# Kernel optimization log

Hardware: AMD Instinct MI355X
Metric: run time of the kernel (lower is better)

## Reference

```python
import jax, jax.numpy as jnp
import numpy as np

# SSMBlock constants (from init_kwargs and standard mamba_ssm defaults)
W = 8            # pooled spatial edge; d_model = W^3
K = 16           # AvgPool3d kernel & stride
D_MODEL = W ** 3            # 512
D_STATE = 16
EXPAND = 2
D_INNER = EXPAND * D_MODEL  # 1024
DT_RANK = D_MODEL // 16     # 32 (ceil(512/16))
D_CONV = 4


def setup_inputs() -> dict:
    key = jax.random.key(0)
    ks = jax.random.split(key, 8)
    s = 0.02
    x = jax.random.normal(ks[0], (1, 64, 128, 128, 128), dtype=jnp.float32)
    in_proj_w = jax.random.normal(ks[1], (2 * D_INNER, D_MODEL), jnp.float32) * s
    conv_w = jax.random.normal(ks[2], (D_INNER, D_CONV), jnp.float32) * s
    conv_b = jnp.zeros((D_INNER,), jnp.float32)
    x_proj_w = jax.random.normal(ks[3], (DT_RANK + 2 * D_STATE, D_INNER), jnp.float32) * s
    dt_proj_w = jax.random.normal(ks[4], (D_INNER, DT_RANK), jnp.float32) * s
    dt_proj_b = jax.random.uniform(ks[5], (D_INNER,), jnp.float32, minval=-4.0, maxval=-2.0)
    A_log = jnp.log(jnp.broadcast_to(jnp.arange(1, D_STATE + 1, dtype=jnp.float32), (D_INNER, D_STATE)))
    D = jnp.ones((D_INNER,), jnp.float32)
    out_proj_w = jax.random.normal(ks[6], (D_MODEL, D_INNER), jnp.float32) * s
    return dict(x=x, in_proj_w=in_proj_w, conv_w=conv_w, conv_b=conv_b,
                x_proj_w=x_proj_w, dt_proj_w=dt_proj_w, dt_proj_b=dt_proj_b,
                A_log=A_log, D=D, out_proj_w=out_proj_w)


def _forward(x, in_proj_w, conv_w, conv_b, x_proj_w, dt_proj_w, dt_proj_b, A_log, D, out_proj_w):
    B, C = x.shape[0], x.shape[1]
    # AvgPool3d(K, stride=K): non-overlapping -> reshape + mean
    xp = x.reshape(B, C, W, K, W, K, W, K).mean(axis=(3, 5, 7))  # (B,C,W,W,W)
    seq = xp.reshape(B, C, D_MODEL)  # Mamba input: L = C, d_model = W^3

    # in_proj -> (x, z)
    xz = jnp.einsum('bld,ed->ble', seq, in_proj_w)  # (B,L,2*D_INNER)
    xs, z = jnp.split(xz, 2, axis=-1)

    # causal depthwise conv1d along L + SiLU
    xt = jnp.pad(xs, ((0, 0), (D_CONV - 1, 0), (0, 0))).transpose(0, 2, 1)  # (B,E,L+pad)
    conv = jax.lax.conv_general_dilated(
        xt, conv_w[:, None, :], window_strides=(1,), padding='VALID',
        dimension_numbers=('NCH', 'OIH', 'NCH'), feature_group_count=D_INNER)
    xs = jax.nn.silu(conv.transpose(0, 2, 1) + conv_b)  # (B,L,E)

    # input-dependent dt, B, C
    x_dbl = jnp.einsum('ble,fe->blf', xs, x_proj_w)
    dt, Bs, Cs = jnp.split(x_dbl, [DT_RANK, DT_RANK + D_STATE], axis=-1)
    dt = jax.nn.softplus(jnp.einsum('blr,er->ble', dt, dt_proj_w) + dt_proj_b)  # (B,L,E)

    # selective scan: h_t = exp(dt*A) h_{t-1} + (dt*x) B_t ; y_t = <h_t, C_t> + D*x_t
    A = -jnp.exp(A_log)                                  # (E,S)
    dA = jnp.exp(dt[..., None] * A)                      # (B,L,E,S)
    dBx = (dt * xs)[..., None] * Bs[:, :, None, :]       # (B,L,E,S)

    def step(h, inp):
        da, dbx, c = inp
        h = da * h + dbx                                 # (B,E,S)
        y = jnp.einsum('bes,bs->be', h, c)
        return h, y

    h0 = jnp.zeros((B, D_INNER, D_STATE), xs.dtype)
    _, ys = jax.lax.scan(step, h0, (dA.transpose(1, 0, 2, 3), dBx.transpose(1, 0, 2, 3), Cs.transpose(1, 0, 2)))
    y = ys.transpose(1, 0, 2) + xs * D                   # (B,L,E)

    y = y * jax.nn.silu(z)
    out = jnp.einsum('ble,de->bld', y, out_proj_w)       # (B,L,d_model)
    return out.reshape(B, C, W, W, W)


def reference(x, in_proj_w, conv_w, conv_b, x_proj_w, dt_proj_w, dt_proj_b, A_log, D, out_proj_w):
    return _forward(x, in_proj_w, conv_w, conv_b, x_proj_w, dt_proj_w, dt_proj_b, A_log, D, out_proj_w)
```

## Files before the change

kernel.cpp:

```cpp
#include <hip/hip_runtime.h>
#include <math.h>

typedef float f32x4 __attribute__((ext_vector_type(4)));

__device__ __forceinline__ float dot4v(f32x4 a, f32x4 b){
    return a.x*b.x + a.y*b.y + a.z*b.z + a.w*b.w;
}
__device__ __forceinline__ float dot4(float4 a, float4 b){
    return a.x*b.x + a.y*b.y + a.z*b.z + a.w*b.w;
}

__device__ __forceinline__ float reduce4(float a0, float a1, float a2, float a3, int lane){
    int b0 = lane & 1, b1 = lane & 2;
    float r  = b0 ? a1 : a0;
    float rt = b0 ? a0 : a1;
    r += __shfl_xor(rt, 1);
    float s  = b0 ? a3 : a2;
    float st = b0 ? a2 : a3;
    s += __shfl_xor(st, 1);
    float u  = b1 ? s : r;
    float ut = b1 ? r : s;
    u += __shfl_xor(ut, 2);
    u += __shfl_xor(u, 4);
    u += __shfl_xor(u, 8);
    u += __shfl_xor(u, 16);
    u += __shfl_xor(u, 32);
    return u;
}

__global__ __launch_bounds__(256) void pool_k(const float* __restrict__ x,
                                              float* __restrict__ seqp){
    int tid  = threadIdx.x;
    int lane = tid & 63;
    int wid  = blockIdx.x * 4 + (tid >> 6);
    int part = wid & 3;
    int cdh  = wid >> 2;
    int c  = cdh >> 6;
    int od = (cdh >> 3) & 7;
    int oh = cdh & 7;
    int half = lane >> 5;
    int f    = lane & 31;

    const f32x4* px = (const f32x4*)x;
    size_t base = ((size_t)(c * 128 + od * 16) * 128 + (size_t)(oh * 16 + half)) * 32 + f
                + (size_t)part * 4 * 4096;

    float acc = 0.f;
    #pragma unroll
    for (int ii = 0; ii < 4; ii++){
        size_t o = base + (size_t)ii * 4096;
        #pragma unroll
        for (int jj = 0; jj < 8; jj++){
            f32x4 v = __builtin_nontemporal_load(&px[o + (size_t)jj * 64]);
            acc += (v.x + v.y) + (v.z + v.w);
        }
    }
    acc += __shfl_xor(acc, 1);
    acc += __shfl_xor(acc, 2);
    acc += __shfl_xor(acc, 32);
    if (lane < 32 && (lane & 3) == 0){
        int ow = lane >> 2;
        seqp[part * 32768 + c * 512 + od * 64 + oh * 8 + ow] = acc * (1.0f / 4096.0f);
    }
}

__device__ __forceinline__ f32x4 loadS(const f32x4* __restrict__ P, int row, int idx){
    f32x4 v = P[(size_t)row * 128 + idx];
    #pragma unroll
    for (int p = 1; p < 4; p++) v += P[(size_t)p * 8192 + (size_t)row * 128 + idx];
    return v;
}

__global__ __launch_bounds__(256) void inproj_k(const float* __restrict__ seqp,
                                                const float* __restrict__ Win,
                                                float* __restrict__ xz){
    int lane = threadIdx.x & 63;
    int wid  = blockIdx.x * 4 + (threadIdx.x >> 6);
    int l0 = (wid >> 7) << 2;
    int e0 = (wid & 127) << 4;
    const f32x4* P = (const f32x4*)seqp;
    f32x4 s0a = loadS(P, l0+0, lane), s0b = loadS(P, l0+0, lane + 64);
    f32x4 s1a = loadS(P, l0+1, lane), s1b = loadS(P, l0+1, lane + 64);
    f32x4 s2a = loadS(P, l0+2, lane), s2b = loadS(P, l0+2, lane + 64);
    f32x4 s3a = loadS(P, l0+3, lane), s3b = loadS(P, l0+3, lane + 64);
    #pragma unroll 4
    for (int j = 0; j < 16; j++){
        int e = e0 + j;
        const f32x4* W = (const f32x4*)Win + (size_t)e * 128;
        f32x4 w0 = W[lane], w1 = W[lane + 64];
        float a0 = dot4v(w0, s0a) + dot4v(w1, s0b);
        float a1 = dot4v(w0, s1a) + dot4v(w1, s1b);
        float a2 = dot4v(w0, s2a) + dot4v(w1, s2b);
        float a3 = dot4v(w0, s3a) + dot4v(w1, s3b);
        float u = reduce4(a0, a1, a2, a3, lane);
        if (lane < 4) xz[(size_t)(l0 + lane) * 2048 + e] = u;
    }
}

__global__ __launch_bounds__(256) void mid_k(const float* __restrict__ xz,
                                             const float* __restrict__ cw,
                                             const float* __restrict__ cb,
                                             const float* __restrict__ Wx,
                                             const float* __restrict__ Wdt,
                                             const float* __restrict__ bdt,
                                             float* __restrict__ xsT,
                                             float* __restrict__ zsT,
                                             float* __restrict__ dtT,
                                             float* __restrict__ bcT){
    __shared__ float xs_row[1024];
    __shared__ float xd_row[64];
    int l = blockIdx.x;
    int t = threadIdx.x;

    #pragma unroll
    for (int j = 0; j < 4; j++){
        int e = t + j * 256;
        float v = cb[e];
        #pragma unroll
        for (int tt = 0; tt < 4; tt++){
            int ll = l - 3 + tt;
            if (ll >= 0) v += cw[e * 4 + tt] * xz[(size_t)ll * 2048 + e];
        }
        v = v / (1.f + expf(-v));
        xs_row[e] = v;
        xsT[(size_t)e * 64 + l] = v;
        float zv = xz[(size_t)l * 2048 + 1024 + e];
        zsT[(size_t)e * 64 + l] = zv / (1.f + expf(-zv));
    }
    __syncthreads();

    {
        int f = t >> 2, q = t & 3;
        const float4* X  = (const float4*)xs_row;
        const float4* W4 = (const float4*)(Wx + (size_t)f * 1024);
        float acc = 0.f;
        #pragma unroll 8
        for (int k = 0; k < 64; k++){
            int idx = q * 64 + k;
            acc += dot4(X[idx], W4[idx]);
        }
        acc += __shfl_xor(acc, 1);
        acc += __shfl_xor(acc, 2);
        if (q == 0){
            xd_row[f] = acc;
            if (f >= 32) bcT[(size_t)(f - 32) * 64 + l] = acc;
        }
    }
    __syncthreads();

    #pragma unroll
    for (int j = 0; j < 4; j++){
        int e = t + j * 256;
        const float4* W4 = (const float4*)(Wdt + (size_t)e * 32);
        const float4* R  = (const float4*)xd_row;
        float acc = bdt[e];
        #pragma unroll
        for (int k4 = 0; k4 < 8; k4++) acc += dot4(R[k4], W4[k4]);
        float sp = (acc > 20.f) ? acc : log1pf(expf(acc));
        dtT[(size_t)e * 64 + l] = sp;
    }
}

__global__ __launch_bounds__(256) void scan_k(const float* __restrict__ dtT,
                                              const float* __restrict__ xsT,
                                              const float* __restrict__ zsT,
                                              const float* __restrict__ bcT,
                                              const float* __restrict__ A_log,
                                              const float* __restrict__ Dv,
                                              float* __restrict__ y){
    __shared__ float red[4][64];
    int e    = blockIdx.x;
    int lane = threadIdx.x & 63;
    int w    = threadIdx.x >> 6;

    float dtv = dtT[(size_t)e * 64 + lane];
    float xv  = xsT[(size_t)e * 64 + lane];

    float py = 0.f;
    #pragma unroll
    for (int i = 0; i < 4; i++){
        int s = w * 4 + i;
        float A = -expf(A_log[e * 16 + s]);
        float a = expf(dtv * A);
        float b = (dtv * xv) * bcT[s * 64 + lane];
        #pragma unroll
        for (int d = 1; d < 64; d <<= 1){
            float ap = __shfl_up(a, d);
            float bp = __shfl_up(b, d);
            if (lane >= d){ b += a * bp; a *= ap; }
        }
        py += b * bcT[(16 + s) * 64 + lane];
    }
    red[w][lane] = py;
    __syncthreads();
    if (threadIdx.x < 64){
        float tot = red[0][lane] + red[1][lane] + red[2][lane] + red[3][lane];
        float yv = (tot + xv * Dv[e]) * zsT[(size_t)e * 64 + lane];
        y[(size_t)lane * 1024 + e] = yv;
    }
}

__global__ __launch_bounds__(256) void outproj_k(const float* __restrict__ y,
                                                 const float* __restrict__ Wo,
                                                 float* __restrict__ out){
    int lane = threadIdx.x & 63;
    int wid  = blockIdx.x * 4 + (threadIdx.x >> 6);
    int l0 = (wid >> 5) << 2;
    int d0 = (wid & 31) << 4;
    const float4* Y = (const float4*)y;
    float4 y0[4], y1[4], y2[4], y3[4];
    #pragma unroll
    for (int q = 0; q < 4; q++){
        y0[q] = Y[(size_t)(l0+0)*256 + q*64 + lane];
        y1[q] = Y[(size_t)(l0+1)*256 + q*64 + lane];
        y2[q] = Y[(size_t)(l0+2)*256 + q*64 + lane];
        y3[q] = Y[(size_t)(l0+3)*256 + q*64 + lane];
    }
    #pragma unroll 2
    for (int j = 0; j < 16; j++){
        int d = d0 + j;
        const float4* W = (const float4*)Wo + (size_t)d * 256;
        float a0 = 0.f, a1 = 0.f, a2 = 0.f, a3 = 0.f;
        #pragma unroll
        for (int q = 0; q < 4; q++){
            float4 w = W[q * 64 + lane];
            a0 += dot4(w, y0[q]);
            a1 += dot4(w, y1[q]);
            a2 += dot4(w, y2[q]);
            a3 += dot4(w, y3[q]);
        }
        float u = reduce4(a0, a1, a2, a3, lane);
        if (lane < 4) out[(size_t)(l0 + lane) * 512 + d] = u;
    }
}

extern "C" void kernel_launch(void* const* d_in, const int* in_sizes, int n_in,
                              void* d_out, int out_size, void* d_ws, size_t ws_size,
                              hipStream_t stream){
    const float* x          = (const float*)d_in[0];
    const float* in_proj_w  = (const float*)d_in[1];
    const float* conv_w     = (const float*)d_in[2];
    const float* conv_b     = (const float*)d_in[3];
    const float* x_proj_w   = (const float*)d_in[4];
    const float* dt_proj_w  = (const float*)d_in[5];
    const float* dt_proj_b  = (const float*)d_in[6];
    const float* A_log      = (const float*)d_in[7];
    const float* Dv         = (const float*)d_in[8];
    const float* out_proj_w = (const float*)d_in[9];
    float* out = (float*)d_out;

    float* ws   = (float*)d_ws;
    float* seqp = ws;
    float* xz   = ws + 131072;
    float* xsT  = ws + 262144;
    float* zsT  = ws + 327680;
    float* dtT  = ws + 393216;
    float* bcT  = ws + 458752;
    float* y    = ws + 460800;

    hipLaunchKernelGGL(pool_k,    dim3(4096), dim3(256), 0, stream, x, seqp);
    hipLaunchKernelGGL(inproj_k,  dim3(512),  dim3(256), 0, stream, seqp, in_proj_w, xz);
    hipLaunchKernelGGL(mid_k,     dim3(64),   dim3(256), 0, stream, xz, conv_w, conv_b,
                       x_proj_w, dt_proj_w, dt_proj_b, xsT, zsT, dtT, bcT);
    hipLaunchKernelGGL(scan_k,    dim3(1024), dim3(256), 0, stream, dtT, xsT, zsT, bcT, A_log, Dv, y);
    hipLaunchKernelGGL(outproj_k, dim3(128),  dim3(256), 0, stream, y, out_proj_w, out);
}
```

Before: 134.7 us.

## Reduce pool partials in-block, widen inproj rows, move dt_proj into scan

```diff
diff --git a/kernel.cpp b/kernel.cpp
--- a/kernel.cpp
+++ b/kernel.cpp
@@ -29,12 +29,12 @@
 }
 
 __global__ __launch_bounds__(256) void pool_k(const float* __restrict__ x,
-                                              float* __restrict__ seqp){
+                                              float* __restrict__ seq){
+    __shared__ float red[4][8];
     int tid  = threadIdx.x;
     int lane = tid & 63;
-    int wid  = blockIdx.x * 4 + (tid >> 6);
-    int part = wid & 3;
-    int cdh  = wid >> 2;
+    int part = tid >> 6;
+    int cdh  = blockIdx.x;
     int c  = cdh >> 6;
     int od = (cdh >> 3) & 7;
     int oh = cdh & 7;
@@ -58,63 +58,59 @@
     acc += __shfl_xor(acc, 1);
     acc += __shfl_xor(acc, 2);
     acc += __shfl_xor(acc, 32);
-    if (lane < 32 && (lane & 3) == 0){
-        int ow = lane >> 2;
-        seqp[part * 32768 + c * 512 + od * 64 + oh * 8 + ow] = acc * (1.0f / 4096.0f);
-    }
-}
-
-__device__ __forceinline__ f32x4 loadS(const f32x4* __restrict__ P, int row, int idx){
-    f32x4 v = P[(size_t)row * 128 + idx];
-    #pragma unroll
-    for (int p = 1; p < 4; p++) v += P[(size_t)p * 8192 + (size_t)row * 128 + idx];
-    return v;
-}
-
-__global__ __launch_bounds__(256) void inproj_k(const float* __restrict__ seqp,
+    if (lane < 32 && (lane & 3) == 0) red[part][lane >> 2] = acc;
+    __syncthreads();
+    if (tid < 8){
+        float v = red[0][tid] + red[1][tid] + red[2][tid] + red[3][tid];
+        seq[c * 512 + od * 64 + oh * 8 + tid] = v * (1.0f / 4096.0f);
+    }
+}
+
+__global__ __launch_bounds__(256) void inproj_k(const float* __restrict__ seq,
                                                 const float* __restrict__ Win,
                                                 float* __restrict__ xz){
     int lane = threadIdx.x & 63;
     int wid  = blockIdx.x * 4 + (threadIdx.x >> 6);
-    int l0 = (wid >> 7) << 2;
+    int l0 = (wid >> 7) << 3;
     int e0 = (wid & 127) << 4;
-    const f32x4* P = (const f32x4*)seqp;
-    f32x4 s0a = loadS(P, l0+0, lane), s0b = loadS(P, l0+0, lane + 64);
-    f32x4 s1a = loadS(P, l0+1, lane), s1b = loadS(P, l0+1, lane + 64);
-    f32x4 s2a = loadS(P, l0+2, lane), s2b = loadS(P, l0+2, lane + 64);
-    f32x4 s3a = loadS(P, l0+3, lane), s3b = loadS(P, l0+3, lane + 64);
-    #pragma unroll 4
+    const f32x4* S = (const f32x4*)seq;
+    f32x4 sa[8], sb[8];
+    #pragma unroll
+    for (int r = 0; r < 8; r++){
+        sa[r] = S[(size_t)(l0 + r) * 128 + lane];
+        sb[r] = S[(size_t)(l0 + r) * 128 + lane + 64];
+    }
+    #pragma unroll 2
     for (int j = 0; j < 16; j++){
         int e = e0 + j;
         const f32x4* W = (const f32x4*)Win + (size_t)e * 128;
         f32x4 w0 = W[lane], w1 = W[lane + 64];
-        float a0 = dot4v(w0, s0a) + dot4v(w1, s0b);
-        float a1 = dot4v(w0, s1a) + dot4v(w1, s1b);
-        float a2 = dot4v(w0, s2a) + dot4v(w1, s2b);
-        float a3 = dot4v(w0, s3a) + dot4v(w1, s3b);
-        float u = reduce4(a0, a1, a2, a3, lane);
-        if (lane < 4) xz[(size_t)(l0 + lane) * 2048 + e] = u;
-    }
-}
-
-__global__ __launch_bounds__(256) void mid_k(const float* __restrict__ xz,
-                                             const float* __restrict__ cw,
-                                             const float* __restrict__ cb,
-                                             const float* __restrict__ Wx,
-                                             const float* __restrict__ Wdt,
-                                             const float* __restrict__ bdt,
-                                             float* __restrict__ xsT,
-                                             float* __restrict__ zsT,
-                                             float* __restrict__ dtT,
-                                             float* __restrict__ bcT){
+        float a[8];
+        #pragma unroll
+        for (int r = 0; r < 8; r++) a[r] = dot4v(w0, sa[r]) + dot4v(w1, sb[r]);
+        float u0 = reduce4(a[0], a[1], a[2], a[3], lane);
+        float u1 = reduce4(a[4], a[5], a[6], a[7], lane);
+        if (lane < 4){
+            xz[(size_t)(l0 + lane) * 2048 + e]     = u0;
+            xz[(size_t)(l0 + 4 + lane) * 2048 + e] = u1;
+        }
+    }
+}
+
+__global__ __launch_bounds__(1024) void cxp_k(const float* __restrict__ xz,
+                                              const float* __restrict__ cw,
+                                              const float* __restrict__ cb,
+                                              const float* __restrict__ Wx,
+                                              float* __restrict__ xsT,
+                                              float* __restrict__ zsT,
+                                              float* __restrict__ bcT,
+                                              float* __restrict__ xdT){
     __shared__ float xs_row[1024];
-    __shared__ float xd_row[64];
     int l = blockIdx.x;
     int t = threadIdx.x;
 
-    #pragma unroll
-    for (int j = 0; j < 4; j++){
-        int e = t + j * 256;
+    {
+        int e = t;
         float v = cb[e];
         #pragma unroll
         for (int tt = 0; tt < 4; tt++){
@@ -130,41 +126,32 @@
     __syncthreads();
 
     {
-        int f = t >> 2, q = t & 3;
+        int f = t >> 4, q = t & 15;
         const float4* X  = (const float4*)xs_row;
         const float4* W4 = (const float4*)(Wx + (size_t)f * 1024);
         float acc = 0.f;
-        #pragma unroll 8
-        for (int k = 0; k < 64; k++){
-            int idx = q * 64 + k;
+        #pragma unroll
+        for (int k4 = 0; k4 < 16; k4++){
+            int idx = q * 16 + k4;
             acc += dot4(X[idx], W4[idx]);
         }
         acc += __shfl_xor(acc, 1);
         acc += __shfl_xor(acc, 2);
+        acc += __shfl_xor(acc, 4);
+        acc += __shfl_xor(acc, 8);
         if (q == 0){
-            xd_row[f] = acc;
-            if (f >= 32) bcT[(size_t)(f - 32) * 64 + l] = acc;
-        }
-    }
-    __syncthreads();
-
-    #pragma unroll
-    for (int j = 0; j < 4; j++){
-        int e = t + j * 256;
-        const float4* W4 = (const float4*)(Wdt + (size_t)e * 32);
-        const float4* R  = (const float4*)xd_row;
-        float acc = bdt[e];
-        #pragma unroll
-        for (int k4 = 0; k4 < 8; k4++) acc += dot4(R[k4], W4[k4]);
-        float sp = (acc > 20.f) ? acc : log1pf(expf(acc));
-        dtT[(size_t)e * 64 + l] = sp;
-    }
-}
-
-__global__ __launch_bounds__(256) void scan_k(const float* __restrict__ dtT,
+            if (f < 32) xdT[(size_t)f * 64 + l] = acc;
+            else        bcT[(size_t)(f - 32) * 64 + l] = acc;
+        }
+    }
+}
+
+__global__ __launch_bounds__(256) void scan_k(const float* __restrict__ xdT,
+                                              const float* __restrict__ bcT,
                                               const float* __restrict__ xsT,
                                               const float* __restrict__ zsT,
-                                              const float* __restrict__ bcT,
+                                              const float* __restrict__ Wdt,
+                                              const float* __restrict__ bdt,
                                               const float* __restrict__ A_log,
                                               const float* __restrict__ Dv,
                                               float* __restrict__ y){
@@ -173,7 +160,10 @@
     int lane = threadIdx.x & 63;
     int w    = threadIdx.x >> 6;
 
-    float dtv = dtT[(size_t)e * 64 + lane];
+    float acc = bdt[e];
+    #pragma unroll 8
+    for (int k = 0; k < 32; k++) acc += xdT[k * 64 + lane] * Wdt[e * 32 + k];
+    float dtv = (acc > 20.f) ? acc : log1pf(expf(acc));
     float xv  = xsT[(size_t)e * 64 + lane];
 
     float py = 0.f;
@@ -250,18 +240,19 @@
     float* out = (float*)d_out;
 
     float* ws   = (float*)d_ws;
-    float* seqp = ws;
-    float* xz   = ws + 131072;
-    float* xsT  = ws + 262144;
-    float* zsT  = ws + 327680;
-    float* dtT  = ws + 393216;
-    float* bcT  = ws + 458752;
-    float* y    = ws + 460800;
-
-    hipLaunchKernelGGL(pool_k,    dim3(4096), dim3(256), 0, stream, x, seqp);
-    hipLaunchKernelGGL(inproj_k,  dim3(512),  dim3(256), 0, stream, seqp, in_proj_w, xz);
-    hipLaunchKernelGGL(mid_k,     dim3(64),   dim3(256), 0, stream, xz, conv_w, conv_b,
-                       x_proj_w, dt_proj_w, dt_proj_b, xsT, zsT, dtT, bcT);
-    hipLaunchKernelGGL(scan_k,    dim3(1024), dim3(256), 0, stream, dtT, xsT, zsT, bcT, A_log, Dv, y);
-    hipLaunchKernelGGL(outproj_k, dim3(128),  dim3(256), 0, stream, y, out_proj_w, out);
-}
+    float* seq  = ws;
+    float* xz   = ws + 32768;
+    float* xsT  = ws + 163840;
+    float* zsT  = ws + 229376;
+    float* bcT  = ws + 294912;
+    float* xdT  = ws + 296960;
+    float* y    = ws + 299008;
+
+    hipLaunchKernelGGL(pool_k,    dim3(4096), dim3(256),  0, stream, x, seq);
+    hipLaunchKernelGGL(inproj_k,  dim3(256),  dim3(256),  0, stream, seq, in_proj_w, xz);
+    hipLaunchKernelGGL(cxp_k,     dim3(64),   dim3(1024), 0, stream, xz, conv_w, conv_b,
+                       x_proj_w, xsT, zsT, bcT, xdT);
+    hipLaunchKernelGGL(scan_k,    dim3(1024), dim3(256),  0, stream, xdT, bcT, xsT, zsT,
+                       dt_proj_w, dt_proj_b, A_log, Dv, y);
+    hipLaunchKernelGGL(outproj_k, dim3(128),  dim3(256),  0, stream, y, out_proj_w, out);
+}
```

After: 126.8 us. 1.06x faster.
